# Kernel optimization log

Hardware: AMD Instinct MI355X
Metric: run time of the kernel (lower is better)

The kernel has to match this reference:

```python
import jax, jax.numpy as jnp
import numpy as np

EPS = 1e-6

def ln2d(x, w, b):
    # LayerNorm over channel dim of NCHW, biased variance, eps=1e-6
    mu = x.mean(1, keepdims=True)
    var = ((x - mu) ** 2).mean(1, keepdims=True)
    y = (x - mu) / jnp.sqrt(var + EPS)
    return w[None, :, None, None] * y + b[None, :, None, None]

def conv1x1(x, w, b):
    # 1x1 conv == pointwise channel mix: w is [C_out, C_in]
    return jnp.einsum('nchw,oc->nohw', x, w) + b[None, :, None, None]

def setup_inputs() -> dict:
    key = jax.random.key(0)
    N, C, H, W = 4, 128, 256, 256
    ks = jax.random.split(key, 8)
    inp = {
        'msi': jax.random.normal(ks[0], (N, C, H, W), jnp.float32),
        'pan': jax.random.normal(ks[1], (N, C, H, W), jnp.float32),
        'ln_w_msi': jnp.ones((C,), jnp.float32),
        'ln_b_msi': jnp.zeros((C,), jnp.float32),
        'ln_w_pan': jnp.ones((C,), jnp.float32),
        'ln_b_pan': jnp.zeros((C,), jnp.float32),
        'w_mp1': jax.random.normal(ks[2], (C, C), jnp.float32) * 0.05,
        'b_mp1': jnp.zeros((C,), jnp.float32),
        'w_pp1': jax.random.normal(ks[3], (C, C), jnp.float32) * 0.05,
        'b_pp1': jnp.zeros((C,), jnp.float32),
        'w_mp2': jax.random.normal(ks[4], (C, C), jnp.float32) * 0.05,
        'b_mp2': jnp.zeros((C,), jnp.float32),
        'w_pp2': jax.random.normal(ks[5], (C, C), jnp.float32) * 0.05,
        'b_pp2': jnp.zeros((C,), jnp.float32),
        'beta': jax.random.normal(ks[6], (1, C, 1, 1), jnp.float32) * 0.1,
        'gamma': jax.random.normal(ks[7], (1, C, 1, 1), jnp.float32) * 0.1,
    }
    return inp

def reference(msi, pan, ln_w_msi, ln_b_msi, ln_w_pan, ln_b_pan,
              w_mp1, b_mp1, w_pp1, b_pp1, w_mp2, b_mp2, w_pp2, b_pp2,
              beta, gamma):
    C = msi.shape[1]
    scale = C ** (-0.5)
    nm = ln2d(msi, ln_w_msi, ln_b_msi)          # norm_msi(msi)
    npn = ln2d(pan, ln_w_pan, ln_b_pan)         # norm_pan(pan)
    q_msi = conv1x1(nm, w_mp1, b_mp1)           # msi_proj1(norm_msi)
    q_pan_from_msi = conv1x1(nm, w_pp1, b_pp1)  # pan_proj1(norm_msi) -- quirk in source
    q_pan = conv1x1(npn, w_pp1, b_pp1)          # pan_proj1(norm_pan)
    v_msi = conv1x1(msi, w_mp2, b_mp2)
    v_pan = conv1x1(pan, w_pp2, b_pp2)
    # per-row attention: contract channels, shared row h -> [N,H,W,W]
    attn_mp = jnp.einsum('nchw,nchv->nhwv', q_msi, q_pan) * scale
    attn_pm = jnp.einsum('nchw,nchv->nhwv', q_pan_from_msi, q_msi) * scale
    f_m2p = jnp.einsum('nhwv,nchv->nchw', jax.nn.softmax(attn_mp, axis=-1), v_pan)
    f_p2m = jnp.einsum('nhwv,nchv->nchw', jax.nn.softmax(attn_pm, axis=-1), v_msi)
    return (msi + f_m2p * beta, pan + f_p2m * gamma)
```

## Files before the change

kernel.cpp:

```cpp
#include <hip/hip_runtime.h>
#include <hip/hip_bf16.h>

typedef __attribute__((ext_vector_type(4))) float f32x4;
typedef __attribute__((ext_vector_type(8))) short s16x8;

#define NB 4
#define CHN 128
#define HH 256
#define WW 256
#define HWSZ (HH*WW)
#define TENSOR_ELEMS ((size_t)NB*CHN*HWSZ)
#define SCALE 0.08838834764831845f

__device__ __forceinline__ unsigned short f2b(float f) {
    unsigned int u = __builtin_bit_cast(unsigned int, f);
    u += 0x7fffu + ((u >> 16) & 1u);
    return (unsigned short)(u >> 16);
}
__device__ __forceinline__ unsigned int pack2(float a, float b) {
    return (unsigned int)f2b(a) | ((unsigned int)f2b(b) << 16);
}
__device__ __forceinline__ float b2f(unsigned int lo16) {
    return __builtin_bit_cast(float, lo16 << 16);
}

__device__ __forceinline__ void stage_w(uint4* bufW4, const float* __restrict__ W, int t) {
    #pragma unroll
    for (int it = 0; it < 4; ++it) {
        int j = it*512 + t;
        int o = j >> 4, ch = j & 15;
        const float4* wp = (const float4*)(W + o*128 + ch*8);
        float4 a = wp[0], b = wp[1];
        uint4 u;
        u.x = pack2(a.x, a.y); u.y = pack2(a.z, a.w);
        u.z = pack2(b.x, b.y); u.w = pack2(b.z, b.w);
        bufW4[o*16 + (ch ^ (o & 7))] = u;
    }
}

__device__ __forceinline__ void gemm_tile(const uint4* bufW4, const uint4* bufB4,
                                          int wave, int lr, int lg, f32x4 acc[8]) {
    s16x8 af[4];
    int arow = wave*16 + lr;
    #pragma unroll
    for (int ks = 0; ks < 4; ++ks)
        af[ks] = __builtin_bit_cast(s16x8, bufW4[arow*16 + ((ks*4+lg) ^ (arow & 7))]);
    #pragma unroll
    for (int nt = 0; nt < 8; ++nt) {
        int brow = nt*16 + lr;
        #pragma unroll
        for (int ks = 0; ks < 4; ++ks) {
            s16x8 bf = __builtin_bit_cast(s16x8, bufB4[brow*16 + ((ks*4+lg) ^ (brow & 7))]);
            acc[nt] = __builtin_amdgcn_mfma_f32_16x16x32_bf16(af[ks], bf, acc[nt], 0, 0, 0);
        }
    }
}

__device__ __forceinline__ void epi_nhwc(unsigned short* __restrict__ out, const float* __restrict__ bias,
                                         int n, int pos0, int wave, int lr, int lg, const f32x4 acc[8]) {
    int cb = wave*16 + lg*4;
    float bs[4];
    #pragma unroll
    for (int r = 0; r < 4; ++r) bs[r] = bias[cb + r];
    #pragma unroll
    for (int nt = 0; nt < 8; ++nt) {
        size_t rowb = ((size_t)n*HWSZ + pos0 + nt*16 + lr)*CHN + cb;
        uint2 u;
        u.x = pack2(acc[nt][0]+bs[0], acc[nt][1]+bs[1]);
        u.y = pack2(acc[nt][2]+bs[2], acc[nt][3]+bs[3]);
        *(uint2*)(out + rowb) = u;
    }
}

__global__ __launch_bounds__(512)
void proj_kernel(const float* __restrict__ msi, const float* __restrict__ pan,
                 const float* __restrict__ lnw_m, const float* __restrict__ lnb_m,
                 const float* __restrict__ lnw_p, const float* __restrict__ lnb_p,
                 const float* __restrict__ w_mp1, const float* __restrict__ b_mp1,
                 const float* __restrict__ w_pp1, const float* __restrict__ b_pp1,
                 const float* __restrict__ w_mp2, const float* __restrict__ b_mp2,
                 const float* __restrict__ w_pp2, const float* __restrict__ b_pp2,
                 unsigned short* __restrict__ ws_u)
{
    __shared__ uint4 pool[4096];
    __shared__ float red[1024];
    __shared__ float s_mu[128];
    __shared__ float s_rs[128];

    uint4* bufB4 = pool;
    uint4* bufW4 = pool + 2048;
    unsigned short* vbounce = (unsigned short*)pool;

    const int t = threadIdx.x;
    const int isPan = blockIdx.y;
    const int gid = blockIdx.x;
    const int n = gid >> 9;
    const int pos0 = (gid & 511) << 7;

    const int pos = t & 127;
    const int cg = t >> 7;

    const float* src = isPan ? pan : msi;
    const float* lnw = isPan ? lnw_p : lnw_m;
    const float* lnb = isPan ? lnb_p : lnb_m;

    unsigned short* q_msi_t = ws_u;
    unsigned short* q_pfm_t = ws_u + TENSOR_ELEMS;
    unsigned short* q_pan_t = ws_u + 2*TENSOR_ELEMS;
    unsigned short* v_msi   = ws_u + 3*TENSOR_ELEMS;
    unsigned short* v_pan   = ws_u + 4*TENSOR_ELEMS;

    float vals[32];
    {
        const float* p = src + ((size_t)(n*CHN + cg*32))*HWSZ + pos0 + pos;
        #pragma unroll
        for (int j = 0; j < 32; ++j) vals[j] = p[(size_t)j*HWSZ];
    }
    #pragma unroll
    for (int k8 = 0; k8 < 4; ++k8) {
        uint4 u;
        u.x = pack2(vals[k8*8+0], vals[k8*8+1]);
        u.y = pack2(vals[k8*8+2], vals[k8*8+3]);
        u.z = pack2(vals[k8*8+4], vals[k8*8+5]);
        u.w = pack2(vals[k8*8+6], vals[k8*8+7]);
        int chunk = cg*4 + k8;
        bufB4[pos*16 + (chunk ^ (pos & 7))] = u;
    }
    stage_w(bufW4, isPan ? w_pp2 : w_mp2, t);
    __syncthreads();

    const int wave = t >> 6, lane = t & 63, lr = lane & 15, lg = lane >> 4;
    const f32x4 zero4 = {0.f, 0.f, 0.f, 0.f};

    f32x4 acc[8];
    #pragma unroll
    for (int i = 0; i < 8; ++i) acc[i] = zero4;
    gemm_tile(bufW4, bufB4, wave, lr, lg, acc);

    float s = 0.f, q = 0.f;
    #pragma unroll
    for (int j = 0; j < 32; ++j) { s += vals[j]; q += vals[j]*vals[j]; }
    red[t] = s; red[512 + t] = q;
    __syncthreads();

    if (t < 128) {
        float S = red[t] + red[t+128] + red[t+256] + red[t+384];
        float Q = red[512+t] + red[512+t+128] + red[512+t+256] + red[512+t+384];
        float mu = S * (1.0f/128.0f);
        float var = Q * (1.0f/128.0f) - mu*mu;
        s_mu[t] = mu;
        s_rs[t] = rsqrtf(var + 1e-6f);
    }
    {
        const float* bias = isPan ? b_pp2 : b_mp2;
        int cb = wave*16 + lg*4;
        float bs[4];
        #pragma unroll
        for (int r = 0; r < 4; ++r) bs[r] = bias[cb + r];
        #pragma unroll
        for (int nt = 0; nt < 8; ++nt) {
            int p = nt*16 + lr;
            #pragma unroll
            for (int r = 0; r < 4; ++r)
                vbounce[(cb + r)*136 + p] = f2b(acc[nt][r] + bs[r]);
        }
    }
    __syncthreads();

    {
        unsigned short* vout = isPan ? v_pan : v_msi;
        #pragma unroll
        for (int i = 0; i < 4; ++i) {
            int fl = i*512 + t;
            int c = fl >> 4, k = fl & 15;
            uint4 u = *(const uint4*)(vbounce + c*136 + k*8);
            *(uint4*)(vout + ((size_t)(n*CHN + c))*HWSZ + pos0 + k*8) = u;
        }
    }
    {
        float mu = s_mu[pos], rs = s_rs[pos];
        #pragma unroll
        for (int j = 0; j < 32; ++j) {
            int c = cg*32 + j;
            vals[j] = (vals[j] - mu) * rs * lnw[c] + lnb[c];
        }
    }
    __syncthreads();

    #pragma unroll
    for (int k8 = 0; k8 < 4; ++k8) {
        uint4 u;
        u.x = pack2(vals[k8*8+0], vals[k8*8+1]);
        u.y = pack2(vals[k8*8+2], vals[k8*8+3]);
        u.z = pack2(vals[k8*8+4], vals[k8*8+5]);
        u.w = pack2(vals[k8*8+6], vals[k8*8+7]);
        int chunk = cg*4 + k8;
        bufB4[pos*16 + (chunk ^ (pos & 7))] = u;
    }
    stage_w(bufW4, isPan ? w_pp1 : w_mp1, t);
    __syncthreads();

    #pragma unroll
    for (int i = 0; i < 8; ++i) acc[i] = zero4;
    gemm_tile(bufW4, bufB4, wave, lr, lg, acc);
    epi_nhwc(isPan ? q_pan_t : q_msi_t, isPan ? b_pp1 : b_mp1, n, pos0, wave, lr, lg, acc);

    if (!isPan) {
        __syncthreads();
        stage_w(bufW4, w_pp1, t);
        __syncthreads();
        #pragma unroll
        for (int i = 0; i < 8; ++i) acc[i] = zero4;
        gemm_tile(bufW4, bufB4, wave, lr, lg, acc);
        epi_nhwc(q_pfm_t, b_pp1, n, pos0, wave, lr, lg, acc);
    }
}

__global__ __launch_bounds__(512, 2)
void attn_kernel(const unsigned short* __restrict__ ws_u,
                 const float* __restrict__ msi, const float* __restrict__ pan,
                 const float* __restrict__ beta, const float* __restrict__ gamma,
                 float* __restrict__ out)
{
    __shared__ uint4 kp4[4096];
    __shared__ uint4 v4[4096];

    const int t = threadIdx.x;
    const int wave = t >> 6, lane = t & 63, lr = lane & 15, lg = lane >> 4;
    const int bid = blockIdx.x;
    const int sib = (bid >> 3) & 3;
    const int nh = (bid >> 5) * 8 + (bid & 7);
    const int path = sib >> 1;
    const int wh = sib & 1;
    const int n = nh >> 8, h = nh & 255;

    const unsigned short* q_msi_t = ws_u;
    const unsigned short* q_pfm_t = ws_u + TENSOR_ELEMS;
    const unsigned short* q_pan_t = ws_u + 2*TENSOR_ELEMS;
    const unsigned short* v_msi   = ws_u + 3*TENSOR_ELEMS;
    const unsigned short* v_pan   = ws_u + 4*TENSOR_ELEMS;

    const unsigned short* Qp = path ? q_pfm_t : q_msi_t;
    const unsigned short* Kp = path ? q_msi_t : q_pan_t;
    const unsigned short* Vp = path ? v_msi   : v_pan;
    const float* resid = path ? pan : msi;
    const float* mul   = path ? gamma : beta;
    float* outp = out + (path ? TENSOR_ELEMS : (size_t)0);

    const size_t qkBase = (size_t)nh * (256*128);
    const unsigned short* vb = Vp + (size_t)n*CHN*HWSZ + (size_t)h*WW;

    {
        const uint4* g = (const uint4*)(Kp + qkBase);
        #pragma unroll
        for (int it = 0; it < 8; ++it) {
            int i = it*512 + t;
            int v = i >> 4, ch = i & 15;
            kp4[v*16 + (ch ^ (v & 7))] = g[i];
        }
    }
    s16x8 qf[4];
    {
        int w = wh*128 + wave*16 + lr;
        const uint4* g = (const uint4*)(Qp + qkBase + (size_t)w*128);
        #pragma unroll
        for (int ks = 0; ks < 4; ++ks) qf[ks] = __builtin_bit_cast(s16x8, g[ks*4 + lg]);
    }
    __syncthreads();

    const f32x4 zero4 = {0.f, 0.f, 0.f, 0.f};
    f32x4 sAcc[16];
    #pragma unroll
    for (int i = 0; i < 16; ++i) sAcc[i] = zero4;
    #pragma unroll
    for (int nt = 0; nt < 16; ++nt) {
        int vrow = nt*16 + lr;
        #pragma unroll
        for (int ks = 0; ks < 4; ++ks) {
            s16x8 kf = __builtin_bit_cast(s16x8, kp4[vrow*16 + ((ks*4+lg) ^ (vrow & 7))]);
            sAcc[nt] = __builtin_amdgcn_mfma_f32_16x16x32_bf16(kf, qf[ks], sAcc[nt], 0, 0, 0);
        }
    }

    {
        #pragma unroll
        for (int it = 0; it < 8; ++it) {
            int i = it*512 + t;
            int c = i >> 5, ch = i & 31;
            const uint4* g = (const uint4*)(vb + (size_t)c*HWSZ + ch*8);
            v4[c*32 + (ch ^ (c & 7))] = g[0];
        }
    }

    f32x4 rsdA[4], rsdB[4];
    {
        const float* rb = resid + (size_t)n*CHN*HWSZ + (size_t)h*WW + wh*128;
        #pragma unroll
        for (int i = 0; i < 4; ++i) {
            int fl = i*512 + t;
            int c = fl >> 4, k = fl & 15;
            const float* p = rb + (size_t)c*HWSZ + k*8;
            rsdA[i] = *(const f32x4*)p;
            rsdB[i] = *(const f32x4*)(p + 4);
        }
    }

    float mx = -1e30f;
    #pragma unroll
    for (int nt = 0; nt < 16; ++nt) {
        #pragma unroll
        for (int r = 0; r < 4; ++r) mx = fmaxf(mx, sAcc[nt][r]);
    }
    mx = fmaxf(mx, __shfl_xor(mx, 16, 64));
    mx = fmaxf(mx, __shfl_xor(mx, 32, 64));
    float sm = 0.f;
    #pragma unroll
    for (int nt = 0; nt < 16; ++nt) {
        #pragma unroll
        for (int r = 0; r < 4; ++r) {
            float p = __expf((sAcc[nt][r] - mx) * SCALE);
            sAcc[nt][r] = p;
            sm += p;
        }
    }
    sm += __shfl_xor(sm, 16, 64);
    sm += __shfl_xor(sm, 32, 64);
    const float inv = 1.0f / sm;

    __syncthreads();

    {
        unsigned short* pbuf = (unsigned short*)kp4;
        const int wloc = wave*16 + lr;
        const int pb_base = wloc*256 + lg*4;
        const int sw = (lr & 7) << 3;
        #pragma unroll
        for (int nt = 0; nt < 16; ++nt) {
            uint2 u;
            u.x = pack2(sAcc[nt][0], sAcc[nt][1]);
            u.y = pack2(sAcc[nt][2], sAcc[nt][3]);
            *(uint2*)(pbuf + ((pb_base + nt*16) ^ sw)) = u;
        }
    }

    f32x4 oAcc[8];
    #pragma unroll
    for (int i = 0; i < 8; ++i) oAcc[i] = zero4;
    const int wrow = wave*16 + lr;
    #pragma unroll
    for (int ks = 0; ks < 8; ++ks) {
        s16x8 pb = __builtin_bit_cast(s16x8, kp4[wrow*32 + ((ks*4+lg) ^ (wrow & 7))]);
        #pragma unroll
        for (int mt = 0; mt < 8; ++mt) {
            int crow = mt*16 + lr;
            s16x8 av = __builtin_bit_cast(s16x8, v4[crow*32 + ((ks*4+lg) ^ (crow & 7))]);
            oAcc[mt] = __builtin_amdgcn_mfma_f32_16x16x32_bf16(av, pb, oAcc[mt], 0, 0, 0);
        }
    }
    __syncthreads();

    {
        unsigned short* obuf = (unsigned short*)kp4;
        int wloc = wave*16 + lr;
        #pragma unroll
        for (int mt = 0; mt < 8; ++mt) {
            int cb = mt*16 + lg*4;
            #pragma unroll
            for (int r = 0; r < 4; ++r)
                obuf[(cb + r)*136 + wloc] = f2b(oAcc[mt][r] * inv);
        }
    }
    __syncthreads();

    {
        const unsigned short* obuf = (const unsigned short*)kp4;
        float* ob = outp + (size_t)n*CHN*HWSZ + (size_t)h*WW + wh*128;
        #pragma unroll
        for (int i = 0; i < 4; ++i) {
            int fl = i*512 + t;
            int c = fl >> 4, k = fl & 15;
            uint4 u = *(const uint4*)(obuf + c*136 + k*8);
            float mc = mul[c];
            f32x4 o0, o1;
            o0[0] = rsdA[i][0] + b2f(u.x & 0xffffu) * mc;
            o0[1] = rsdA[i][1] + b2f(u.x >> 16) * mc;
            o0[2] = rsdA[i][2] + b2f(u.y & 0xffffu) * mc;
            o0[3] = rsdA[i][3] + b2f(u.y >> 16) * mc;
            o1[0] = rsdB[i][0] + b2f(u.z & 0xffffu) * mc;
            o1[1] = rsdB[i][1] + b2f(u.z >> 16) * mc;
            o1[2] = rsdB[i][2] + b2f(u.w & 0xffffu) * mc;
            o1[3] = rsdB[i][3] + b2f(u.w >> 16) * mc;
            float* p = ob + (size_t)c*HWSZ + k*8;
            *(f32x4*)p = o0;
            *(f32x4*)(p + 4) = o1;
        }
    }
}

extern "C" void kernel_launch(void* const* d_in, const int* in_sizes, int n_in,
                              void* d_out, int out_size, void* d_ws, size_t ws_size,
                              hipStream_t stream) {
    (void)in_sizes; (void)n_in; (void)out_size; (void)ws_size;
    const float* msi   = (const float*)d_in[0];
    const float* pan   = (const float*)d_in[1];
    const float* lnw_m = (const float*)d_in[2];
    const float* lnb_m = (const float*)d_in[3];
    const float* lnw_p = (const float*)d_in[4];
    const float* lnb_p = (const float*)d_in[5];
    const float* w_mp1 = (const float*)d_in[6];
    const float* b_mp1 = (const float*)d_in[7];
    const float* w_pp1 = (const float*)d_in[8];
    const float* b_pp1 = (const float*)d_in[9];
    const float* w_mp2 = (const float*)d_in[10];
    const float* b_mp2 = (const float*)d_in[11];
    const float* w_pp2 = (const float*)d_in[12];
    const float* b_pp2 = (const float*)d_in[13];
    const float* beta  = (const float*)d_in[14];
    const float* gamma = (const float*)d_in[15];
    unsigned short* ws_u = (unsigned short*)d_ws;
    float* out = (float*)d_out;

    proj_kernel<<<dim3(2048, 2), 512, 0, stream>>>(
        msi, pan, lnw_m, lnb_m, lnw_p, lnb_p,
        w_mp1, b_mp1, w_pp1, b_pp1, w_mp2, b_mp2, w_pp2, b_pp2, ws_u);
    attn_kernel<<<dim3(4096), 512, 0, stream>>>(
        ws_u, msi, pan, beta, gamma, out);
}
```

Before: 393.4 us.

## Process both query halves per block to reuse K and V tiles

Each attention block now handles all 256 query columns of a row (two 128-wide halves) instead of one half, halving the grid and sharing the staged K and V tiles in LDS across both halves. This removes the duplicated global loads of K and V that two sibling blocks previously did. The softmax exponent is also switched to exp2f with a pre-folded log2(e)*scale constant. In exchange, register pressure roughly doubles (two sets of Q fragments, packed probabilities and output accumulators), which may spill or cut occupancy under the 512x2 launch bounds. Residual loads also move to the epilogue, so they are no longer issued early to overlap with compute.

```diff
diff --git a/kernel.cpp b/kernel.cpp
--- a/kernel.cpp
+++ b/kernel.cpp
@@ -11,6 +11,7 @@
 #define HWSZ (HH*WW)
 #define TENSOR_ELEMS ((size_t)NB*CHN*HWSZ)
 #define SCALE 0.08838834764831845f
+#define SC2 0.12751889550584484f
 
 __device__ __forceinline__ unsigned short f2b(float f) {
     unsigned int u = __builtin_bit_cast(unsigned int, f);
@@ -228,10 +229,8 @@
     const int t = threadIdx.x;
     const int wave = t >> 6, lane = t & 63, lr = lane & 15, lg = lane >> 4;
     const int bid = blockIdx.x;
-    const int sib = (bid >> 3) & 3;
-    const int nh = (bid >> 5) * 8 + (bid & 7);
-    const int path = sib >> 1;
-    const int wh = sib & 1;
+    const int path = (bid >> 3) & 1;
+    const int nh = (bid >> 4) * 8 + (bid & 7);
     const int n = nh >> 8, h = nh & 255;
 
     const unsigned short* q_msi_t = ws_u;
@@ -259,17 +258,22 @@
             kp4[v*16 + (ch ^ (v & 7))] = g[i];
         }
     }
-    s16x8 qf[4];
-    {
-        int w = wh*128 + wave*16 + lr;
-        const uint4* g = (const uint4*)(Qp + qkBase + (size_t)w*128);
-        #pragma unroll
-        for (int ks = 0; ks < 4; ++ks) qf[ks] = __builtin_bit_cast(s16x8, g[ks*4 + lg]);
+    s16x8 qf0[4], qf1[4];
+    {
+        int w = wave*16 + lr;
+        const uint4* g0 = (const uint4*)(Qp + qkBase + (size_t)w*128);
+        const uint4* g1 = (const uint4*)(Qp + qkBase + (size_t)(w + 128)*128);
+        #pragma unroll
+        for (int ks = 0; ks < 4; ++ks) {
+            qf0[ks] = __builtin_bit_cast(s16x8, g0[ks*4 + lg]);
+            qf1[ks] = __builtin_bit_cast(s16x8, g1[ks*4 + lg]);
+        }
     }
     __syncthreads();
 
     const f32x4 zero4 = {0.f, 0.f, 0.f, 0.f};
     f32x4 sAcc[16];
+
     #pragma unroll
     for (int i = 0; i < 16; ++i) sAcc[i] = zero4;
     #pragma unroll
@@ -278,7 +282,7 @@
         #pragma unroll
         for (int ks = 0; ks < 4; ++ks) {
             s16x8 kf = __builtin_bit_cast(s16x8, kp4[vrow*16 + ((ks*4+lg) ^ (vrow & 7))]);
-            sAcc[nt] = __builtin_amdgcn_mfma_f32_16x16x32_bf16(kf, qf[ks], sAcc[nt], 0, 0, 0);
+            sAcc[nt] = __builtin_amdgcn_mfma_f32_16x16x32_bf16(kf, qf0[ks], sAcc[nt], 0, 0, 0);
         }
     }
 
@@ -292,61 +296,93 @@
         }
     }
 
-    f32x4 rsdA[4], rsdB[4];
-    {
-        const float* rb = resid + (size_t)n*CHN*HWSZ + (size_t)h*WW + wh*128;
-        #pragma unroll
-        for (int i = 0; i < 4; ++i) {
-            int fl = i*512 + t;
-            int c = fl >> 4, k = fl & 15;
-            const float* p = rb + (size_t)c*HWSZ + k*8;
-            rsdA[i] = *(const f32x4*)p;
-            rsdB[i] = *(const f32x4*)(p + 4);
-        }
-    }
-
-    float mx = -1e30f;
+    float inv0;
+    uint2 pk0[16];
+    {
+        float mx = -1e30f;
+        #pragma unroll
+        for (int nt = 0; nt < 16; ++nt) {
+            #pragma unroll
+            for (int r = 0; r < 4; ++r) mx = fmaxf(mx, sAcc[nt][r]);
+        }
+        mx = fmaxf(mx, __shfl_xor(mx, 16, 64));
+        mx = fmaxf(mx, __shfl_xor(mx, 32, 64));
+        float sm = 0.f;
+        #pragma unroll
+        for (int nt = 0; nt < 16; ++nt) {
+            #pragma unroll
+            for (int r = 0; r < 4; ++r) {
+                float p = exp2f((sAcc[nt][r] - mx) * SC2);
+                sAcc[nt][r] = p;
+                sm += p;
+            }
+        }
+        sm += __shfl_xor(sm, 16, 64);
+        sm += __shfl_xor(sm, 32, 64);
+        inv0 = 1.0f / sm;
+        #pragma unroll
+        for (int nt = 0; nt < 16; ++nt) {
+            pk0[nt].x = pack2(sAcc[nt][0], sAcc[nt][1]);
+            pk0[nt].y = pack2(sAcc[nt][2], sAcc[nt][3]);
+        }
+    }
+
+    #pragma unroll
+    for (int i = 0; i < 16; ++i) sAcc[i] = zero4;
     #pragma unroll
     for (int nt = 0; nt < 16; ++nt) {
-        #pragma unroll
-        for (int r = 0; r < 4; ++r) mx = fmaxf(mx, sAcc[nt][r]);
-    }
-    mx = fmaxf(mx, __shfl_xor(mx, 16, 64));
-    mx = fmaxf(mx, __shfl_xor(mx, 32, 64));
-    float sm = 0.f;
-    #pragma unroll
-    for (int nt = 0; nt < 16; ++nt) {
-        #pragma unroll
-        for (int r = 0; r < 4; ++r) {
-            float p = __expf((sAcc[nt][r] - mx) * SCALE);
-            sAcc[nt][r] = p;
-            sm += p;
-        }
-    }
-    sm += __shfl_xor(sm, 16, 64);
-    sm += __shfl_xor(sm, 32, 64);
-    const float inv = 1.0f / sm;
-
-    __syncthreads();
-
-    {
-        unsigned short* pbuf = (unsigned short*)kp4;
-        const int wloc = wave*16 + lr;
-        const int pb_base = wloc*256 + lg*4;
-        const int sw = (lr & 7) << 3;
-        #pragma unroll
-        for (int nt = 0; nt < 16; ++nt) {
-            uint2 u;
-            u.x = pack2(sAcc[nt][0], sAcc[nt][1]);
-            u.y = pack2(sAcc[nt][2], sAcc[nt][3]);
-            *(uint2*)(pbuf + ((pb_base + nt*16) ^ sw)) = u;
-        }
-    }
-
-    f32x4 oAcc[8];
-    #pragma unroll
-    for (int i = 0; i < 8; ++i) oAcc[i] = zero4;
+        int vrow = nt*16 + lr;
+        #pragma unroll
+        for (int ks = 0; ks < 4; ++ks) {
+            s16x8 kf = __builtin_bit_cast(s16x8, kp4[vrow*16 + ((ks*4+lg) ^ (vrow & 7))]);
+            sAcc[nt] = __builtin_amdgcn_mfma_f32_16x16x32_bf16(kf, qf1[ks], sAcc[nt], 0, 0, 0);
+        }
+    }
+    float inv1;
+    uint2 pk1[16];
+    {
+        float mx = -1e30f;
+        #pragma unroll
+        for (int nt = 0; nt < 16; ++nt) {
+            #pragma unroll
+            for (int r = 0; r < 4; ++r) mx = fmaxf(mx, sAcc[nt][r]);
+        }
+        mx = fmaxf(mx, __shfl_xor(mx, 16, 64));
+        mx = fmaxf(mx, __shfl_xor(mx, 32, 64));
+        float sm = 0.f;
+        #pragma unroll
+        for (int nt = 0; nt < 16; ++nt) {
+            #pragma unroll
+            for (int r = 0; r < 4; ++r) {
+                float p = exp2f((sAcc[nt][r] - mx) * SC2);
+                sAcc[nt][r] = p;
+                sm += p;
+            }
+        }
+        sm += __shfl_xor(sm, 16, 64);
+        sm += __shfl_xor(sm, 32, 64);
+        inv1 = 1.0f / sm;
+        #pragma unroll
+        for (int nt = 0; nt < 16; ++nt) {
+            pk1[nt].x = pack2(sAcc[nt][0], sAcc[nt][1]);
+            pk1[nt].y = pack2(sAcc[nt][2], sAcc[nt][3]);
+        }
+    }
+
+    __syncthreads();
+
+    unsigned short* pbuf = (unsigned short*)kp4;
+    const int wloc = wave*16 + lr;
+    const int pb_base = wloc*256 + lg*4;
+    const int sw = (lr & 7) << 3;
     const int wrow = wave*16 + lr;
+
+    #pragma unroll
+    for (int nt = 0; nt < 16; ++nt)
+        *(uint2*)(pbuf + ((pb_base + nt*16) ^ sw)) = pk0[nt];
+    f32x4 oAcc0[8];
+    #pragma unroll
+    for (int i = 0; i < 8; ++i) oAcc0[i] = zero4;
     #pragma unroll
     for (int ks = 0; ks < 8; ++ks) {
         s16x8 pb = __builtin_bit_cast(s16x8, kp4[wrow*32 + ((ks*4+lg) ^ (wrow & 7))]);
@@ -354,45 +390,71 @@
         for (int mt = 0; mt < 8; ++mt) {
             int crow = mt*16 + lr;
             s16x8 av = __builtin_bit_cast(s16x8, v4[crow*32 + ((ks*4+lg) ^ (crow & 7))]);
-            oAcc[mt] = __builtin_amdgcn_mfma_f32_16x16x32_bf16(av, pb, oAcc[mt], 0, 0, 0);
-        }
-    }
-    __syncthreads();
-
-    {
-        unsigned short* obuf = (unsigned short*)kp4;
-        int wloc = wave*16 + lr;
+            oAcc0[mt] = __builtin_amdgcn_mfma_f32_16x16x32_bf16(av, pb, oAcc0[mt], 0, 0, 0);
+        }
+    }
+    #pragma unroll
+    for (int nt = 0; nt < 16; ++nt)
+        *(uint2*)(pbuf + ((pb_base + nt*16) ^ sw)) = pk1[nt];
+    f32x4 oAcc1[8];
+    #pragma unroll
+    for (int i = 0; i < 8; ++i) oAcc1[i] = zero4;
+    #pragma unroll
+    for (int ks = 0; ks < 8; ++ks) {
+        s16x8 pb = __builtin_bit_cast(s16x8, kp4[wrow*32 + ((ks*4+lg) ^ (wrow & 7))]);
+        #pragma unroll
+        for (int mt = 0; mt < 8; ++mt) {
+            int crow = mt*16 + lr;
+            s16x8 av = __builtin_bit_cast(s16x8, v4[crow*32 + ((ks*4+lg) ^ (crow & 7))]);
+            oAcc1[mt] = __builtin_amdgcn_mfma_f32_16x16x32_bf16(av, pb, oAcc1[mt], 0, 0, 0);
+        }
+    }
+    __syncthreads();
+
+    {
+        unsigned short* ob0 = (unsigned short*)kp4;
+        unsigned short* ob1 = (unsigned short*)v4;
         #pragma unroll
         for (int mt = 0; mt < 8; ++mt) {
             int cb = mt*16 + lg*4;
             #pragma unroll
-            for (int r = 0; r < 4; ++r)
-                obuf[(cb + r)*136 + wloc] = f2b(oAcc[mt][r] * inv);
-        }
-    }
-    __syncthreads();
-
-    {
-        const unsigned short* obuf = (const unsigned short*)kp4;
-        float* ob = outp + (size_t)n*CHN*HWSZ + (size_t)h*WW + wh*128;
-        #pragma unroll
-        for (int i = 0; i < 4; ++i) {
-            int fl = i*512 + t;
-            int c = fl >> 4, k = fl & 15;
-            uint4 u = *(const uint4*)(obuf + c*136 + k*8);
-            float mc = mul[c];
-            f32x4 o0, o1;
-            o0[0] = rsdA[i][0] + b2f(u.x & 0xffffu) * mc;
-            o0[1] = rsdA[i][1] + b2f(u.x >> 16) * mc;
-            o0[2] = rsdA[i][2] + b2f(u.y & 0xffffu) * mc;
-            o0[3] = rsdA[i][3] + b2f(u.y >> 16) * mc;
-            o1[0] = rsdB[i][0] + b2f(u.z & 0xffffu) * mc;
-            o1[1] = rsdB[i][1] + b2f(u.z >> 16) * mc;
-            o1[2] = rsdB[i][2] + b2f(u.w & 0xffffu) * mc;
-            o1[3] = rsdB[i][3] + b2f(u.w >> 16) * mc;
-            float* p = ob + (size_t)c*HWSZ + k*8;
-            *(f32x4*)p = o0;
-            *(f32x4*)(p + 4) = o1;
+            for (int r = 0; r < 4; ++r) {
+                ob0[(cb + r)*136 + wloc] = f2b(oAcc0[mt][r] * inv0);
+                ob1[(cb + r)*136 + wloc] = f2b(oAcc1[mt][r] * inv1);
+            }
+        }
+    }
+    __syncthreads();
+
+    {
+        const float* rb = resid + (size_t)n*CHN*HWSZ + (size_t)h*WW;
+        float* ob = outp + (size_t)n*CHN*HWSZ + (size_t)h*WW;
+        #pragma unroll
+        for (int half = 0; half < 2; ++half) {
+            const unsigned short* obuf = (const unsigned short*)(half ? v4 : kp4);
+            int woff = half * 128;
+            #pragma unroll
+            for (int i = 0; i < 4; ++i) {
+                int fl = i*512 + t;
+                int c = fl >> 4, k = fl & 15;
+                const float* rp = rb + (size_t)c*HWSZ + woff + k*8;
+                f32x4 rA = *(const f32x4*)rp;
+                f32x4 rB = *(const f32x4*)(rp + 4);
+                uint4 u = *(const uint4*)(obuf + c*136 + k*8);
+                float mc = mul[c];
+                f32x4 o0, o1;
+                o0[0] = rA[0] + b2f(u.x & 0xffffu) * mc;
+                o0[1] = rA[1] + b2f(u.x >> 16) * mc;
+                o0[2] = rA[2] + b2f(u.y & 0xffffu) * mc;
+                o0[3] = rA[3] + b2f(u.y >> 16) * mc;
+                o1[0] = rB[0] + b2f(u.z & 0xffffu) * mc;
+                o1[1] = rB[1] + b2f(u.z >> 16) * mc;
+                o1[2] = rB[2] + b2f(u.w & 0xffffu) * mc;
+                o1[3] = rB[3] + b2f(u.w >> 16) * mc;
+                float* p = ob + (size_t)c*HWSZ + woff + k*8;
+                *(f32x4*)p = o0;
+                *(f32x4*)(p + 4) = o1;
+            }
         }
     }
 }
@@ -423,6 +485,6 @@
     proj_kernel<<<dim3(2048, 2), 512, 0, stream>>>(
         msi, pan, lnw_m, lnb_m, lnw_p, lnb_p,
         w_mp1, b_mp1, w_pp1, b_pp1, w_mp2, b_mp2, w_pp2, b_pp2, ws_u);
-    attn_kernel<<<dim3(4096), 512, 0, stream>>>(
+    attn_kernel<<<dim3(2048), 512, 0, stream>>>(
         ws_u, msi, pan, beta, gamma, out);
 }
```

New measurement: 406.2 us. +3.3%, slower.
